# Optimization experiments

Hardware: AMD Instinct MI355X
Metric: run time of the kernel (lower is better)

## Reference

```python
import math
import jax, jax.numpy as jnp
import numpy as np

B, T, D, H, L = 8, 512, 128, 128, 2
W_SCALE = 0.05  # xavier-like small init to keep exp() input gate numerically sane


def setup_inputs() -> dict:
    key = jax.random.key(0)
    ks = jax.random.split(key, 14)
    inp = {"x": jax.random.normal(ks[0], (B, T, D), jnp.float32)}
    names_w = ["Wq", "Wk", "Wv", "Wi", "Wf", "Wo"]
    for j, nm in enumerate(names_w):
        inp[nm] = jax.random.normal(ks[1 + j], (L, H, D), jnp.float32) * W_SCALE
    # q/k/v biases zero-initialized per reset_parameters; gate biases random
    inp["bq"] = jnp.zeros((L, H), jnp.float32)
    inp["bk"] = jnp.zeros((L, H), jnp.float32)
    inp["bv"] = jnp.zeros((L, H), jnp.float32)
    inp["bi"] = jax.random.normal(ks[7], (L, H), jnp.float32) * W_SCALE
    inp["bf"] = jax.random.normal(ks[8], (L, H), jnp.float32) * W_SCALE
    inp["bo"] = jax.random.normal(ks[9], (L, H), jnp.float32) * W_SCALE
    return inp


def _mlstm_layer(xin, Wq, bq, Wk, bk, Wv, bv, Wi, bi, Wf, bf, Wo, bo):
    # xin: (B, T, Din). Precompute all 6 projections for the full sequence.
    q = jnp.einsum("btd,hd->bth", xin, Wq) + bq
    k = (jnp.einsum("btd,hd->bth", xin, Wk) + bk) * (1.0 / math.sqrt(H))
    v = jnp.einsum("btd,hd->bth", xin, Wv) + bv
    i = jnp.exp(jnp.einsum("btd,hd->bth", xin, Wi) + bi)
    f = jax.nn.sigmoid(jnp.einsum("btd,hd->bth", xin, Wf) + bf)
    o = jax.nn.sigmoid(jnp.einsum("btd,hd->bth", xin, Wo) + bo)

    def step(carry, qkvifo):
        C, n = carry                      # C: (B,H,H), n: (B,H)
        qt, kt, vt, it, ft, ot = qkvifo   # each (B,H)
        h_tilde = jnp.einsum("bij,bj->bi", C, qt)
        denom = jnp.maximum(jnp.abs(jnp.einsum("bi,bi->b", n, qt)), 1.0)[:, None]
        h = ot * (h_tilde / denom)
        n_new = ft * n + it * kt
        C_new = ft[:, :, None] * C + it[:, :, None] * (vt[:, :, None] * kt[:, None, :])
        return (C_new, n_new), h

    Bc = xin.shape[0]
    C0 = jnp.zeros((Bc, H, H), xin.dtype)
    n0 = jnp.zeros((Bc, H), xin.dtype)
    seq = tuple(jnp.swapaxes(a, 0, 1) for a in (q, k, v, i, f, o))  # (T,B,H)
    _, hs = jax.lax.scan(step, (C0, n0), seq)
    return jnp.swapaxes(hs, 0, 1)  # (B,T,H)


def reference(x, Wq, bq, Wk, bk, Wv, bv, Wi, bi, Wf, bf, Wo, bo):
    h = x
    for l in range(L):  # small fixed layer loop (dropout=0.0 -> identity)
        h = _mlstm_layer(h, Wq[l], bq[l], Wk[l], bk[l], Wv[l], bv[l],
                         Wi[l], bi[l], Wf[l], bf[l], Wo[l], bo[l])
    return h  # (B, T, H) output sequence of last layer
```

## Files before the change

### kernel.cpp

```cpp
#include <hip/hip_runtime.h>
#include <math.h>

#define BB 8
#define TT 512
#define DD 128
#define HH 128
#define BT_ (BB * TT)
#define CL 32
#define NCH 16
static const size_t BTH = (size_t)BT_ * HH;


struct WArgs { const float* W[6]; };
struct BArgs { const float* b[6]; };

template <int CTRL>
__device__ __forceinline__ float dpp_add(float x) {
  int y = __builtin_amdgcn_update_dpp(0, __builtin_bit_cast(int, x), CTRL,
                                      0xF, 0xF, true);
  return x + __builtin_bit_cast(float, y);
}

__global__ __launch_bounds__(256)
void transpose_w(WArgs w, float* __restrict__ Wt) {
  __shared__ float t[32][33];
  const int l = blockIdx.y / 6, p = blockIdx.y % 6;
  const float* src = w.W[p] + (size_t)l * HH * DD;
  float* dst = Wt + (size_t)blockIdx.y * HH * DD;
  const int ty0 = (blockIdx.x >> 2) * 32, tx0 = (blockIdx.x & 3) * 32;
  const int tx = threadIdx.x & 31, ty = threadIdx.x >> 5;
#pragma unroll
  for (int j = 0; j < 32; j += 8)
    t[ty + j][tx] = src[(size_t)(ty0 + ty + j) * DD + tx0 + tx];
  __syncthreads();
#pragma unroll
  for (int j = 0; j < 32; j += 8)
    dst[(size_t)(tx0 + ty + j) * HH + ty0 + tx] = t[tx][ty + j];
}

__global__ __launch_bounds__(256)
void proj_kernel(const float* __restrict__ X, const float* __restrict__ Wtl,
                 BArgs args, float* __restrict__ act) {
  __shared__ float xs[32][132];
  const int p = blockIdx.y;
  const int row0 = blockIdx.x * 32;
  const int tid = threadIdx.x;
  {
    const float4* xg = (const float4*)(X + (size_t)row0 * DD);
#pragma unroll
    for (int i = 0; i < 4; ++i) {
      int u = tid + 256 * i;
      float4 v = xg[u];
      *(float4*)&xs[u >> 5][(u & 31) * 4] = v;
    }
  }
  __syncthreads();

  const int h0 = (tid & 15) * 8;
  const int r0 = (tid >> 4) * 2;
  const float* wtp = Wtl + (size_t)p * HH * DD;

  float acc[2][8];
#pragma unroll
  for (int r = 0; r < 2; ++r)
#pragma unroll
    for (int j = 0; j < 8; ++j) acc[r][j] = 0.f;

  for (int d0 = 0; d0 < DD; d0 += 4) {
    float4 wa[4], wb[4];
#pragma unroll
    for (int i = 0; i < 4; ++i) {
      wa[i] = *(const float4*)(wtp + (size_t)(d0 + i) * HH + h0);
      wb[i] = *(const float4*)(wtp + (size_t)(d0 + i) * HH + h0 + 4);
    }
    float4 x0 = *(const float4*)&xs[r0][d0];
    float4 x1 = *(const float4*)&xs[r0 + 1][d0];
    const float xa[4] = {x0.x, x0.y, x0.z, x0.w};
    const float xb[4] = {x1.x, x1.y, x1.z, x1.w};
#pragma unroll
    for (int i = 0; i < 4; ++i) {
      acc[0][0] = fmaf(xa[i], wa[i].x, acc[0][0]);
      acc[0][1] = fmaf(xa[i], wa[i].y, acc[0][1]);
      acc[0][2] = fmaf(xa[i], wa[i].z, acc[0][2]);
      acc[0][3] = fmaf(xa[i], wa[i].w, acc[0][3]);
      acc[0][4] = fmaf(xa[i], wb[i].x, acc[0][4]);
      acc[0][5] = fmaf(xa[i], wb[i].y, acc[0][5]);
      acc[0][6] = fmaf(xa[i], wb[i].z, acc[0][6]);
      acc[0][7] = fmaf(xa[i], wb[i].w, acc[0][7]);
      acc[1][0] = fmaf(xb[i], wa[i].x, acc[1][0]);
      acc[1][1] = fmaf(xb[i], wa[i].y, acc[1][1]);
      acc[1][2] = fmaf(xb[i], wa[i].z, acc[1][2]);
      acc[1][3] = fmaf(xb[i], wa[i].w, acc[1][3]);
      acc[1][4] = fmaf(xb[i], wb[i].x, acc[1][4]);
      acc[1][5] = fmaf(xb[i], wb[i].y, acc[1][5]);
      acc[1][6] = fmaf(xb[i], wb[i].z, acc[1][6]);
      acc[1][7] = fmaf(xb[i], wb[i].w, acc[1][7]);
    }
  }

  const float4 b0 = *(const float4*)(args.b[p] + h0);
  const float4 b1 = *(const float4*)(args.b[p] + h0 + 4);
  const float bias[8] = {b0.x, b0.y, b0.z, b0.w, b1.x, b1.y, b1.z, b1.w};
#pragma unroll
  for (int r = 0; r < 2; ++r) {
    const size_t row = (size_t)row0 + r0 + r;
    float v[8];
#pragma unroll
    for (int j = 0; j < 8; ++j) {
      float a = acc[r][j] + bias[j];
      if (p == 1)      a *= 0.088388347648318447f;
      else if (p == 3) a = __expf(a);
      else if (p >= 4) a = 1.0f / (1.0f + __expf(-a));
      v[j] = a;
    }
    if (p == 0) {
      float* dst = act + row * HH + h0;
      *(float4*)dst = make_float4(v[0], v[1], v[2], v[3]);
      *(float4*)(dst + 4) = make_float4(v[4], v[5], v[6], v[7]);
    } else if (p == 1) {
      float* dst = act + BTH + row * HH + h0;
      *(float4*)dst = make_float4(v[0], v[1], v[2], v[3]);
      *(float4*)(dst + 4) = make_float4(v[4], v[5], v[6], v[7]);
    } else if (p == 3 || p == 4) {
      float* dst = act + 2 * BTH + row * 2 * HH + 2 * h0 + (p == 3 ? 0 : 1);
#pragma unroll
      for (int j = 0; j < 8; ++j) dst[2 * j] = v[j];
    } else {
      float* dst = act + 4 * BTH + row * 2 * HH + 2 * h0 + (p == 2 ? 0 : 1);
#pragma unroll
      for (int j = 0; j < 8; ++j) dst[2 * j] = v[j];
    }
  }
}

__global__ __launch_bounds__(512)
void cseg2_kernel(const float* __restrict__ act, float* __restrict__ cbuf,
                  float* __restrict__ abuf, float* __restrict__ nbufB) {
  __shared__ __align__(16) float kt[CL][128];
  __shared__ __align__(16) float ift[CL][64];
  __shared__ __align__(16) float vot[CL][64];
  const int tid = threadIdx.x;
  const int lane = tid & 63, wid = tid >> 6;
  const int blk = blockIdx.x;
  const int b = blk & 7, ch = (blk >> 3) & (NCH - 1), qtr = blk >> 7;
  const int t0 = ch * CL;
  const int p0 = qtr * 32;
  const size_t boff = (size_t)b * TT * HH;
  const float* kg = act + BTH + boff;
  const float* ifg = act + 2 * BTH + 2 * boff;
  const float* vog = act + 4 * BTH + 2 * boff;

#pragma unroll
  for (int i = 0; i < CL / 16; ++i) {
    const int u = tid + 512 * i;
    const int r = u >> 5, c = (u & 31) * 4;
    *(float4*)&kt[r][c] = *(const float4*)(kg + (size_t)(t0 + r) * HH + c);
  }
  {
    const int r = tid >> 4, c = (tid & 15) * 4;
    *(float4*)&ift[r][c] =
        *(const float4*)(ifg + (size_t)(t0 + r) * 2 * HH + 2 * p0 + c);
    *(float4*)&vot[r][c] =
        *(const float4*)(vog + (size_t)(t0 + r) * 2 * HH + 2 * p0 + c);
  }
  __syncthreads();

  const int pl = lane >> 4, cl = lane & 15;
  const int plocal = wid * 4 + pl;
  const int p = p0 + plocal;

  float C[8];
#pragma unroll
  for (int j = 0; j < 8; ++j) C[j] = 0.f;
  float Af = 1.f, Bn = 0.f;

#pragma unroll 4
  for (int t = 0; t < CL; ++t) {
    const float2 gif = *(const float2*)&ift[t][2 * plocal];
    const float2 gvo = *(const float2*)&vot[t][2 * plocal];
    const float4 k0 = *(const float4*)&kt[t][cl * 4];
    const float4 k1 = *(const float4*)&kt[t][cl * 4 + 64];
    const float kp = kt[t][p];
    const float a = gif.x * gvo.x;
    const float f = gif.y;
    C[0] = fmaf(f, C[0], a * k0.x);
    C[1] = fmaf(f, C[1], a * k0.y);
    C[2] = fmaf(f, C[2], a * k0.z);
    C[3] = fmaf(f, C[3], a * k0.w);
    C[4] = fmaf(f, C[4], a * k1.x);
    C[5] = fmaf(f, C[5], a * k1.y);
    C[6] = fmaf(f, C[6], a * k1.z);
    C[7] = fmaf(f, C[7], a * k1.w);
    Af *= f;
    Bn = fmaf(f, Bn, gif.x * kp);
  }

  const size_t slot = (size_t)(b * 128 + p) * NCH + ch;
  *(float4*)(cbuf + slot * 128 + cl * 4) = make_float4(C[0], C[1], C[2], C[3]);
  *(float4*)(cbuf + slot * 128 + cl * 4 + 64) =
      make_float4(C[4], C[5], C[6], C[7]);
  if (cl == 0) {
    abuf[slot] = Af;
    nbufB[slot] = Bn;
  }
}

__global__ __launch_bounds__(128)
void ndenom_kernel(float* __restrict__ act, const float* __restrict__ abuf,
                   const float* __restrict__ nbufB) {
  __shared__ float plds[8][132];
  __shared__ float den[8];
  const int b = blockIdx.x & 7, ch = blockIdx.x >> 3;
  const int p = threadIdx.x;
  const size_t boff = (size_t)b * TT * HH;
  const float* qp = act + boff + p;
  const float* kp = act + BTH + boff + p;
  const float* ifp = act + 2 * BTH + 2 * boff + 2 * p;
  float* vop = act + 4 * BTH + 2 * boff;
  const size_t cb = (size_t)(b * 128 + p) * NCH;

  float n = 0.f;
#pragma unroll 1
  for (int g = 0; g < ch; ++g) n = fmaf(abuf[cb + g], n, nbufB[cb + g]);

#pragma unroll 1
  for (int grp = 0; grp < CL / 8; ++grp) {
    const int t0 = ch * CL + grp * 8;
    float prod[8];
#pragma unroll
    for (int j = 0; j < 8; ++j) {
      const float2 iff = *(const float2*)(ifp + (size_t)(t0 + j) * 2 * HH);
      const float kv = kp[(size_t)(t0 + j) * HH];
      const float qv = qp[(size_t)(t0 + j) * HH];
      prod[j] = n * qv;
      n = fmaf(iff.y, n, iff.x * kv);
    }
#pragma unroll
    for (int j = 0; j < 8; ++j) plds[j][p] = prod[j];
    __syncthreads();
    {
      const int j = p >> 4, c = p & 15;
      const float4 a = *(const float4*)&plds[j][c * 8];
      const float4 d = *(const float4*)&plds[j][c * 8 + 4];
      float s = ((a.x + a.y) + (a.z + a.w)) + ((d.x + d.y) + (d.z + d.w));
      s = dpp_add<0x111>(s);
      s = dpp_add<0x112>(s);
      s = dpp_add<0x114>(s);
      s = dpp_add<0x118>(s);
      if ((p & 15) == 15)
        den[j] = __builtin_amdgcn_rcpf(fmaxf(fabsf(s), 1.0f));
    }
    __syncthreads();
#pragma unroll
    for (int j = 0; j < 8; ++j)
      vop[(size_t)(t0 + j) * 2 * HH + 2 * p + 1] *= den[j];
  }
}

__global__ __launch_bounds__(512)
void hscan2_kernel(const float* __restrict__ act, float* __restrict__ hout,
                   const float* __restrict__ cbuf,
                   const float* __restrict__ abuf) {
  __shared__ __align__(16) float qt[CL][128];
  __shared__ __align__(16) float kt[CL][128];
  __shared__ __align__(16) float ift[CL][64];
  __shared__ __align__(16) float vot[CL][64];
  const int tid = threadIdx.x;
  const int lane = tid & 63, wid = tid >> 6;
  const int blk = blockIdx.x;
  const int b = blk & 7, ch = (blk >> 3) & (NCH - 1), qtr = blk >> 7;
  const int t0 = ch * CL;
  const int p0 = qtr * 32;
  const size_t boff = (size_t)b * TT * HH;
  const float* qg = act + boff;
  const float* kg = act + BTH + boff;
  const float* ifg = act + 2 * BTH + 2 * boff;
  const float* vog = act + 4 * BTH + 2 * boff;

#pragma unroll
  for (int i = 0; i < CL / 16; ++i) {
    const int u = tid + 512 * i;
    const int r = u >> 5, c = (u & 31) * 4;
    *(float4*)&qt[r][c] = *(const float4*)(qg + (size_t)(t0 + r) * HH + c);
    *(float4*)&kt[r][c] = *(const float4*)(kg + (size_t)(t0 + r) * HH + c);
  }
  {
    const int r = tid >> 4, c = (tid & 15) * 4;
    *(float4*)&ift[r][c] =
        *(const float4*)(ifg + (size_t)(t0 + r) * 2 * HH + 2 * p0 + c);
    *(float4*)&vot[r][c] =
        *(const float4*)(vog + (size_t)(t0 + r) * 2 * HH + 2 * p0 + c);
  }
  __syncthreads();

  const int pl = lane >> 4, cl = lane & 15;
  const int plocal = wid * 4 + pl;
  const int p = p0 + plocal;

  float C[8];
#pragma unroll
  for (int j = 0; j < 8; ++j) C[j] = 0.f;
  {
    const size_t cb = (size_t)(b * 128 + p) * NCH;
#pragma unroll 1
    for (int g = 0; g < ch; ++g) {
      const float a = abuf[cb + g];
      const float4 b0 = *(const float4*)(cbuf + (cb + g) * 128 + cl * 4);
      const float4 b1 = *(const float4*)(cbuf + (cb + g) * 128 + cl * 4 + 64);
      C[0] = fmaf(a, C[0], b0.x);
      C[1] = fmaf(a, C[1], b0.y);
      C[2] = fmaf(a, C[2], b0.z);
      C[3] = fmaf(a, C[3], b0.w);
      C[4] = fmaf(a, C[4], b1.x);
      C[5] = fmaf(a, C[5], b1.y);
      C[6] = fmaf(a, C[6], b1.z);
      C[7] = fmaf(a, C[7], b1.w);
    }
  }
  float* hbase = hout + boff + p;

#pragma unroll 4
  for (int t = 0; t < CL; ++t) {
    const float2 gif = *(const float2*)&ift[t][2 * plocal];
    const float2 gvo = *(const float2*)&vot[t][2 * plocal];
    const float4 q0 = *(const float4*)&qt[t][cl * 4];
    const float4 q1 = *(const float4*)&qt[t][cl * 4 + 64];
    const float4 k0 = *(const float4*)&kt[t][cl * 4];
    const float4 k1 = *(const float4*)&kt[t][cl * 4 + 64];
    float s0 = C[0] * q0.x;
    float s1 = C[4] * q1.x;
    s0 = fmaf(C[1], q0.y, s0);
    s1 = fmaf(C[5], q1.y, s1);
    s0 = fmaf(C[2], q0.z, s0);
    s1 = fmaf(C[6], q1.z, s1);
    s0 = fmaf(C[3], q0.w, s0);
    s1 = fmaf(C[7], q1.w, s1);
    float s = s0 + s1;
    const float a = gif.x * gvo.x;
    const float f = gif.y;
    C[0] = fmaf(f, C[0], a * k0.x);
    C[1] = fmaf(f, C[1], a * k0.y);
    C[2] = fmaf(f, C[2], a * k0.z);
    C[3] = fmaf(f, C[3], a * k0.w);
    C[4] = fmaf(f, C[4], a * k1.x);
    C[5] = fmaf(f, C[5], a * k1.y);
    C[6] = fmaf(f, C[6], a * k1.z);
    C[7] = fmaf(f, C[7], a * k1.w);
    s = dpp_add<0x111>(s);
    s = dpp_add<0x112>(s);
    s = dpp_add<0x114>(s);
    s = dpp_add<0x118>(s);
    if (cl == 15) hbase[(size_t)(t0 + t) * HH] = s * gvo.y;
  }
}

extern "C" void kernel_launch(void* const* d_in, const int* in_sizes, int n_in,
                              void* d_out, int out_size, void* d_ws,
                              size_t ws_size, hipStream_t stream) {
  (void)in_sizes; (void)n_in; (void)out_size; (void)ws_size;
  const float* x = (const float*)d_in[0];
  float* act = (float*)d_ws;
  float* hbuf = act + 6 * BTH;
  float* cbuf = act + 7 * BTH;
  float* abuf = cbuf + (size_t)1024 * NCH * 128;
  float* nbufB = abuf + (size_t)1024 * NCH;
  float* Wt = (float*)d_out;

  WArgs wa;
  for (int j = 0; j < 6; ++j) wa.W[j] = (const float*)d_in[1 + j];
  transpose_w<<<dim3(16, 12), 256, 0, stream>>>(wa, Wt);

  for (int l = 0; l < 2; ++l) {
    BArgs ba;
    for (int j = 0; j < 6; ++j)
      ba.b[j] = (const float*)d_in[7 + j] + (size_t)l * HH;
    const float* wtl = Wt + (size_t)l * 6 * HH * DD;
    const float* xin = (l == 0) ? x : hbuf;
    float* hdst = (l == 0) ? hbuf : (float*)d_out;
    proj_kernel<<<dim3(BT_ / 32, 6), 256, 0, stream>>>(xin, wtl, ba, act);
    cseg2_kernel<<<512, 512, 0, stream>>>(act, cbuf, abuf, nbufB);
    ndenom_kernel<<<128, 128, 0, stream>>>(act, abuf, nbufB);
    hscan2_kernel<<<512, 512, 0, stream>>>(act, hdst, cbuf, abuf);
  }
}
```

Before: 216.7 us.

## Fuse chunk scan, denominator and output scan into one cooperative kernel

Replaces the three per-layer scan kernels (chunk-state build, normalizer/denominator, output scan) with a single cooperative kernel that uses grid-wide syncs between phases. The q/k/gate tiles are loaded into shared memory once and reused across phases. The normalizer scan is parallelized over 64 eight-step segments per batch using per-segment affine summaries instead of a serial pass in 128 blocks. It also removes two launches per layer, at the cost of grid barriers and requiring 512 co-resident blocks. If cooperative launch fails it falls back to the old kernels.

```diff
diff --git a/kernel.cpp b/kernel.cpp
--- a/kernel.cpp
+++ b/kernel.cpp
@@ -1,5 +1,8 @@
 #include <hip/hip_runtime.h>
+#include <hip/hip_cooperative_groups.h>
 #include <math.h>
+
+namespace cg = cooperative_groups;
 
 #define BB 8
 #define TT 512
@@ -133,6 +136,205 @@
   }
 }
 
+__global__ __launch_bounds__(512, 4)
+void scanfused_kernel(const float* __restrict__ act, float* __restrict__ hout,
+                      float* __restrict__ cbuf, float* __restrict__ abuf,
+                      float* __restrict__ segA, float* __restrict__ segBn,
+                      float* __restrict__ denb) {
+  __shared__ __align__(16) float qt[CL][128];
+  __shared__ __align__(16) float kt[CL][128];
+  __shared__ __align__(16) float ift[CL][64];
+  __shared__ __align__(16) float vot[CL][64];
+  __shared__ float plds[8][132];
+  __shared__ float dlds[CL];
+  cg::grid_group grid = cg::this_grid();
+
+  const int tid = threadIdx.x;
+  const int lane = tid & 63, wid = tid >> 6;
+  const int blk = blockIdx.x;
+  const int b = blk & 7, ch = (blk >> 3) & (NCH - 1), qtr = blk >> 7;
+  const int t0 = ch * CL;
+  const int p0 = qtr * 32;
+  const size_t boff = (size_t)b * TT * HH;
+  const float* qg = act + boff;
+  const float* kg = act + BTH + boff;
+  const float* ifg = act + 2 * BTH + 2 * boff;
+  const float* vog = act + 4 * BTH + 2 * boff;
+
+#pragma unroll
+  for (int i = 0; i < CL / 16; ++i) {
+    const int u = tid + 512 * i;
+    const int r = u >> 5, c = (u & 31) * 4;
+    *(float4*)&qt[r][c] = *(const float4*)(qg + (size_t)(t0 + r) * HH + c);
+    *(float4*)&kt[r][c] = *(const float4*)(kg + (size_t)(t0 + r) * HH + c);
+  }
+  {
+    const int r = tid >> 4, c = (tid & 15) * 4;
+    *(float4*)&ift[r][c] =
+        *(const float4*)(ifg + (size_t)(t0 + r) * 2 * HH + 2 * p0 + c);
+    *(float4*)&vot[r][c] =
+        *(const float4*)(vog + (size_t)(t0 + r) * 2 * HH + 2 * p0 + c);
+  }
+  __syncthreads();
+
+  const int pl = lane >> 4, cl = lane & 15;
+  const int plocal = wid * 4 + pl;
+  const int p = p0 + plocal;
+
+  {
+    float C[8];
+#pragma unroll
+    for (int j = 0; j < 8; ++j) C[j] = 0.f;
+    float Af = 1.f, Aw = 1.f, Bw = 0.f;
+#pragma unroll 4
+    for (int t = 0; t < CL; ++t) {
+      const float2 gif = *(const float2*)&ift[t][2 * plocal];
+      const float2 gvo = *(const float2*)&vot[t][2 * plocal];
+      const float4 k0 = *(const float4*)&kt[t][cl * 4];
+      const float4 k1 = *(const float4*)&kt[t][cl * 4 + 64];
+      const float kp = kt[t][p];
+      const float a = gif.x * gvo.x;
+      const float f = gif.y;
+      C[0] = fmaf(f, C[0], a * k0.x);
+      C[1] = fmaf(f, C[1], a * k0.y);
+      C[2] = fmaf(f, C[2], a * k0.z);
+      C[3] = fmaf(f, C[3], a * k0.w);
+      C[4] = fmaf(f, C[4], a * k1.x);
+      C[5] = fmaf(f, C[5], a * k1.y);
+      C[6] = fmaf(f, C[6], a * k1.z);
+      C[7] = fmaf(f, C[7], a * k1.w);
+      Af *= f;
+      Aw *= f;
+      Bw = fmaf(f, Bw, gif.x * kp);
+      if ((t & 7) == 7) {
+        if (cl == 0) {
+          const size_t ss = ((size_t)(b * 64) + ch * 4 + (t >> 3)) * 128 + p;
+          segA[ss] = Aw;
+          segBn[ss] = Bw;
+        }
+        Aw = 1.f;
+        Bw = 0.f;
+      }
+    }
+    const size_t slot = (size_t)(b * 128 + p) * NCH + ch;
+    *(float4*)(cbuf + slot * 128 + cl * 4) =
+        make_float4(C[0], C[1], C[2], C[3]);
+    *(float4*)(cbuf + slot * 128 + cl * 4 + 64) =
+        make_float4(C[4], C[5], C[6], C[7]);
+    if (cl == 0) abuf[slot] = Af;
+  }
+
+  grid.sync();
+
+  {
+    const int b2 = blk & 7, seg = blk >> 3;
+    const int tB0 = seg * 8;
+    if (tid < 128) {
+      const int p2 = tid;
+      const size_t boff2 = (size_t)b2 * TT * HH;
+      const float* qp2 = act + boff2 + p2;
+      const float* kp2 = act + BTH + boff2 + p2;
+      const float* ifp2 = act + 2 * BTH + 2 * boff2 + 2 * p2;
+      const size_t sb = (size_t)(b2 * 64) * 128 + p2;
+      float n = 0.f;
+#pragma unroll 1
+      for (int g = 0; g < seg; ++g)
+        n = fmaf(segA[sb + (size_t)g * 128], n, segBn[sb + (size_t)g * 128]);
+      float prod[8];
+#pragma unroll
+      for (int j = 0; j < 8; ++j) {
+        const float2 iff = *(const float2*)(ifp2 + (size_t)(tB0 + j) * 2 * HH);
+        const float kv = kp2[(size_t)(tB0 + j) * HH];
+        const float qv = qp2[(size_t)(tB0 + j) * HH];
+        prod[j] = n * qv;
+        n = fmaf(iff.y, n, iff.x * kv);
+      }
+#pragma unroll
+      for (int j = 0; j < 8; ++j) plds[j][p2] = prod[j];
+    }
+    __syncthreads();
+    if (tid < 128) {
+      const int p2 = tid;
+      const int j = p2 >> 4, c = p2 & 15;
+      const float4 a = *(const float4*)&plds[j][c * 8];
+      const float4 d = *(const float4*)&plds[j][c * 8 + 4];
+      float s = ((a.x + a.y) + (a.z + a.w)) + ((d.x + d.y) + (d.z + d.w));
+      s = dpp_add<0x111>(s);
+      s = dpp_add<0x112>(s);
+      s = dpp_add<0x114>(s);
+      s = dpp_add<0x118>(s);
+      if ((p2 & 15) == 15)
+        denb[(size_t)(b2 << 9) + tB0 + j] =
+            __builtin_amdgcn_rcpf(fmaxf(fabsf(s), 1.0f));
+    }
+  }
+
+  grid.sync();
+
+  if (tid < CL) dlds[tid] = denb[(size_t)(b << 9) + t0 + tid];
+  __syncthreads();
+  {
+    const int u = tid, u2 = tid + 512;
+    vot[u >> 5][2 * (u & 31) + 1] *= dlds[u >> 5];
+    vot[u2 >> 5][2 * (u2 & 31) + 1] *= dlds[u2 >> 5];
+  }
+  __syncthreads();
+  {
+    float C[8];
+#pragma unroll
+    for (int j = 0; j < 8; ++j) C[j] = 0.f;
+    const size_t cb = (size_t)(b * 128 + p) * NCH;
+#pragma unroll 1
+    for (int g = 0; g < ch; ++g) {
+      const float a = abuf[cb + g];
+      const float4 b0 = *(const float4*)(cbuf + (cb + g) * 128 + cl * 4);
+      const float4 b1 = *(const float4*)(cbuf + (cb + g) * 128 + cl * 4 + 64);
+      C[0] = fmaf(a, C[0], b0.x);
+      C[1] = fmaf(a, C[1], b0.y);
+      C[2] = fmaf(a, C[2], b0.z);
+      C[3] = fmaf(a, C[3], b0.w);
+      C[4] = fmaf(a, C[4], b1.x);
+      C[5] = fmaf(a, C[5], b1.y);
+      C[6] = fmaf(a, C[6], b1.z);
+      C[7] = fmaf(a, C[7], b1.w);
+    }
+    float* hbase = hout + boff + p;
+#pragma unroll 4
+    for (int t = 0; t < CL; ++t) {
+      const float2 gif = *(const float2*)&ift[t][2 * plocal];
+      const float2 gvo = *(const float2*)&vot[t][2 * plocal];
+      const float4 q0 = *(const float4*)&qt[t][cl * 4];
+      const float4 q1 = *(const float4*)&qt[t][cl * 4 + 64];
+      const float4 k0 = *(const float4*)&kt[t][cl * 4];
+      const float4 k1 = *(const float4*)&kt[t][cl * 4 + 64];
+      float s0 = C[0] * q0.x;
+      float s1 = C[4] * q1.x;
+      s0 = fmaf(C[1], q0.y, s0);
+      s1 = fmaf(C[5], q1.y, s1);
+      s0 = fmaf(C[2], q0.z, s0);
+      s1 = fmaf(C[6], q1.z, s1);
+      s0 = fmaf(C[3], q0.w, s0);
+      s1 = fmaf(C[7], q1.w, s1);
+      float s = s0 + s1;
+      const float a = gif.x * gvo.x;
+      const float f = gif.y;
+      C[0] = fmaf(f, C[0], a * k0.x);
+      C[1] = fmaf(f, C[1], a * k0.y);
+      C[2] = fmaf(f, C[2], a * k0.z);
+      C[3] = fmaf(f, C[3], a * k0.w);
+      C[4] = fmaf(f, C[4], a * k1.x);
+      C[5] = fmaf(f, C[5], a * k1.y);
+      C[6] = fmaf(f, C[6], a * k1.z);
+      C[7] = fmaf(f, C[7], a * k1.w);
+      s = dpp_add<0x111>(s);
+      s = dpp_add<0x112>(s);
+      s = dpp_add<0x114>(s);
+      s = dpp_add<0x118>(s);
+      if (cl == 15) hbase[(size_t)(t0 + t) * HH] = s * gvo.y;
+    }
+  }
+}
+
 __global__ __launch_bounds__(512)
 void cseg2_kernel(const float* __restrict__ act, float* __restrict__ cbuf,
                   float* __restrict__ abuf, float* __restrict__ nbufB) {
@@ -173,7 +375,6 @@
 #pragma unroll
   for (int j = 0; j < 8; ++j) C[j] = 0.f;
   float Af = 1.f, Bn = 0.f;
-
 #pragma unroll 4
   for (int t = 0; t < CL; ++t) {
     const float2 gif = *(const float2*)&ift[t][2 * plocal];
@@ -194,7 +395,6 @@
     Af *= f;
     Bn = fmaf(f, Bn, gif.x * kp);
   }
-
   const size_t slot = (size_t)(b * 128 + p) * NCH + ch;
   *(float4*)(cbuf + slot * 128 + cl * 4) = make_float4(C[0], C[1], C[2], C[3]);
   *(float4*)(cbuf + slot * 128 + cl * 4 + 64) =
@@ -363,7 +563,10 @@
   float* hbuf = act + 6 * BTH;
   float* cbuf = act + 7 * BTH;
   float* abuf = cbuf + (size_t)1024 * NCH * 128;
-  float* nbufB = abuf + (size_t)1024 * NCH;
+  float* segA = abuf + (size_t)1024 * NCH;
+  float* segBn = segA + 65536;
+  float* denb = segBn + 65536;
+  float* nbufB = denb + 4096;
   float* Wt = (float*)d_out;
 
   WArgs wa;
@@ -378,8 +581,18 @@
     const float* xin = (l == 0) ? x : hbuf;
     float* hdst = (l == 0) ? hbuf : (float*)d_out;
     proj_kernel<<<dim3(BT_ / 32, 6), 256, 0, stream>>>(xin, wtl, ba, act);
-    cseg2_kernel<<<512, 512, 0, stream>>>(act, cbuf, abuf, nbufB);
-    ndenom_kernel<<<128, 128, 0, stream>>>(act, abuf, nbufB);
-    hscan2_kernel<<<512, 512, 0, stream>>>(act, hdst, cbuf, abuf);
-  }
-}
+
+    const float* actc = act;
+    float* hd = hdst;
+    void* kargs[] = {(void*)&actc, (void*)&hd,    (void*)&cbuf, (void*)&abuf,
+                     (void*)&segA, (void*)&segBn, (void*)&denb};
+    hipError_t e = hipLaunchCooperativeKernel(
+        (const void*)&scanfused_kernel, dim3(512), dim3(512), kargs, 0,
+        stream);
+    if (e != hipSuccess) {
+      cseg2_kernel<<<512, 512, 0, stream>>>(act, cbuf, abuf, nbufB);
+      ndenom_kernel<<<128, 128, 0, stream>>>(act, abuf, nbufB);
+      hscan2_kernel<<<512, 512, 0, stream>>>(act, hdst, cbuf, abuf);
+    }
+  }
+}
```

After: 442.1 us. +104.0%, slower.
